# Performance work log

Hardware: AMD Instinct MI355X
Metric: run time of the kernel (lower is better)

Reference implementation:

```python
import jax, jax.numpy as jnp
import numpy as np

N = 50000
F_IN = 256
D_HID = 64
H = 8
C = 10
E_RAND = 800000
ALPHA = 0.2  # leaky_relu negative slope


def setup_inputs() -> dict:
    key = jax.random.key(0)
    k = jax.random.split(key, 7)
    x = jax.random.normal(k[0], (N, F_IN), dtype=jnp.float32)
    # edge list = self-loops (ensure nonzero softmax denominator) + random edges
    self_idx = jnp.arange(N, dtype=jnp.int32)
    edge_src = jnp.concatenate([self_idx, jax.random.randint(k[1], (E_RAND,), 0, N, dtype=jnp.int32)])
    edge_dst = jnp.concatenate([self_idx, jax.random.randint(k[2], (E_RAND,), 0, N, dtype=jnp.int32)])
    W_heads = jax.random.normal(k[3], (H, F_IN, D_HID), dtype=jnp.float32) * 0.05
    a_heads = jax.random.normal(k[4], (H, 2 * D_HID), dtype=jnp.float32) * 0.05
    W_out = jax.random.normal(k[5], (H * D_HID, C), dtype=jnp.float32) * 0.05
    a_out = jax.random.normal(k[6], (2 * C,), dtype=jnp.float32) * 0.05
    return {"x": x, "edge_src": edge_src, "edge_dst": edge_dst,
            "W_heads": W_heads, "a_heads": a_heads, "W_out": W_out, "a_out": a_out}


def sp_gat_layer(x, W, a, src, dst, concat):
    """pyGAT SpGraphAttentionLayer (eval mode, dropout off)."""
    n = x.shape[0]
    d = W.shape[1]
    h = x @ W                                             # [N, d]
    score = h[src] @ a[:d] + h[dst] @ a[d:]               # [E] per-edge attention logit
    e = jnp.exp(-jax.nn.leaky_relu(score, ALPHA))         # unnormalized attention
    rowsum = jax.ops.segment_sum(e, src, num_segments=n)  # [N] softmax denominator
    agg = jax.ops.segment_sum(e[:, None] * h[dst], src, num_segments=n)  # [N, d]
    out = agg / rowsum[:, None]
    return jax.nn.elu(out) if concat else out


def reference(x, edge_src, edge_dst, W_heads, a_heads, W_out, a_out):
    # multi-head sparse attention, heads concatenated along feature dim
    heads = jax.vmap(lambda W, a: sp_gat_layer(x, W, a, edge_src, edge_dst, True))(W_heads, a_heads)  # [H, N, d]
    xcat = jnp.transpose(heads, (1, 0, 2)).reshape(x.shape[0], -1)  # [N, H*d]
    out = jax.nn.elu(sp_gat_layer(xcat, W_out, a_out, edge_src, edge_dst, False))  # [N, C]
    return jax.nn.log_softmax(out, axis=1)
```

## Files before the change

kernel.cpp:

```cpp
#include <hip/hip_runtime.h>
#include <hip/hip_bf16.h>

#define F_IN    256
#define D_HID   64
#define H_HEADS 8
#define NC      10
#define ALPHA   0.2f
#define FLAG_THRESH 64
#define SCAN_T  1024

typedef __attribute__((ext_vector_type(8))) short short8;
typedef __attribute__((ext_vector_type(4))) float f32x4;

__device__ __forceinline__ float bfu2f(unsigned short u) {
    union { float f; unsigned int i; } c; c.i = ((unsigned int)u) << 16; return c.f;
}
__device__ __forceinline__ unsigned short f2bfu(float f) {
    union { float f; unsigned int i; } c; c.f = f;
    unsigned int x = c.i;
    x += 0x7fffu + ((x >> 16) & 1u);
    return (unsigned short)(x >> 16);
}

__global__ void detect_kernel(const unsigned int* __restrict__ x, int* __restrict__ flag) {
    int t = threadIdx.x;
    int cnt = 0;
    for (int i = t; i < 4096; i += 256) {
        unsigned int w = x[i];
        unsigned int e = (w >> 7) & 0xffu;
        if (e >= 140u) cnt++;
    }
    atomicAdd(flag, cnt);
}

__global__ __launch_bounds__(256) void prep_kernel(
    const void* __restrict__ x_raw,  unsigned short* __restrict__ x_bf,
    const void* __restrict__ Wh_raw, unsigned short* __restrict__ wh_t,
    const void* __restrict__ ah_raw, float* __restrict__ ah32,
    const void* __restrict__ Wo_raw, float* __restrict__ Wo32,
    const void* __restrict__ ao_raw, float* __restrict__ ao32,
    const int* __restrict__ esrc, int* __restrict__ counts,
    const int* __restrict__ flagp, int N, int E,
    int bx, int bw, int ba, int bo)
{
    int b = blockIdx.x;
    bool isf32 = (*flagp > FLAG_THRESH);
    if (b < bx) {
        long i = (long)b * 256 + threadIdx.x;
        long n8 = (long)N * F_IN / 8;
        if (i < n8) {
            unsigned short o[8];
            if (isf32) {
                const float* s = (const float*)x_raw + i * 8;
                #pragma unroll
                for (int j = 0; j < 8; ++j) o[j] = f2bfu(s[j]);
            } else {
                *(uint4*)o = ((const uint4*)x_raw)[i];
            }
            *(uint4*)(x_bf + i * 8) = *(uint4*)o;
        }
    } else if (b < bw) {
        int i = (b - bx) * 256 + threadIdx.x;
        int d = i & 63, k = (i >> 6) & 255, h = i >> 14;
        float v = isf32 ? ((const float*)Wh_raw)[i] : bfu2f(((const unsigned short*)Wh_raw)[i]);
        wh_t[(h * 64 + d) * 256 + k] = f2bfu(v);
    } else if (b < ba) {
        int i = (b - bw) * 256 + threadIdx.x;
        ah32[i] = isf32 ? ((const float*)ah_raw)[i] : bfu2f(((const unsigned short*)ah_raw)[i]);
    } else if (b < bo) {
        int i = (b - ba) * 256 + threadIdx.x;
        Wo32[i] = isf32 ? ((const float*)Wo_raw)[i] : bfu2f(((const unsigned short*)Wo_raw)[i]);
    } else if (b == bo) {
        int i = threadIdx.x;
        if (i < 2 * NC)
            ao32[i] = isf32 ? ((const float*)ao_raw)[i] : bfu2f(((const unsigned short*)ao_raw)[i]);
    } else {
        int e = (b - bo - 1) * 256 + threadIdx.x;
        if (e < E) atomicAdd(&counts[esrc[e]], 1);
    }
}

__global__ __launch_bounds__(SCAN_T) void scan_kernel(
    const int* __restrict__ counts, int* __restrict__ row_start, int N, int E)
{
    __shared__ int sums[SCAN_T];
    int t = threadIdx.x;
    int chunk = (N + SCAN_T - 1) / SCAN_T;
    int b = t * chunk, e = min(b + chunk, N);
    int s = 0;
    for (int i = b; i < e; ++i) s += counts[i];
    sums[t] = s;
    __syncthreads();
    for (int off = 1; off < SCAN_T; off <<= 1) {
        int u = (t >= off) ? sums[t - off] : 0;
        __syncthreads();
        sums[t] += u;
        __syncthreads();
    }
    int running = sums[t] - s;
    for (int i = b; i < e; ++i) { row_start[i] = running; running += counts[i]; }
    if (t == SCAN_T - 1) row_start[N] = E;
}

__global__ __launch_bounds__(256) void scatter_ev_kernel(
    const int* __restrict__ src, const int* __restrict__ dst,
    const int* __restrict__ row_start, int* __restrict__ cursor,
    const float* __restrict__ s1s, const float* __restrict__ s1d,
    int* __restrict__ csr_dst, float* __restrict__ ev_csr, int E)
{
    int e = blockIdx.x * 256 + threadIdx.x;
    if (e >= E) return;
    int s = src[e], d = dst[e];
    int pos = atomicAdd(&cursor[s], 1);
    int i = row_start[s] + pos;
    csr_dst[i] = d;
    float4 ss0 = *(const float4*)(s1s + s * 8);
    float4 ss1 = *(const float4*)(s1s + s * 8 + 4);
    float4 sd0 = *(const float4*)(s1d + d * 8);
    float4 sd1 = *(const float4*)(s1d + d * 8 + 4);
    float sc[8] = { ss0.x + sd0.x, ss0.y + sd0.y, ss0.z + sd0.z, ss0.w + sd0.w,
                    ss1.x + sd1.x, ss1.y + sd1.y, ss1.z + sd1.z, ss1.w + sd1.w };
    float ev[8];
    #pragma unroll
    for (int h = 0; h < 8; ++h) {
        float lr = sc[h] > 0.f ? sc[h] : ALPHA * sc[h];
        ev[h] = __expf(-lr);
    }
    *(float4*)(ev_csr + (long)i * 8)     = make_float4(ev[0], ev[1], ev[2], ev[3]);
    *(float4*)(ev_csr + (long)i * 8 + 4) = make_float4(ev[4], ev[5], ev[6], ev[7]);
}

__global__ __launch_bounds__(256) void gemm1_kernel(
    const unsigned short* __restrict__ x_bf,
    const unsigned short* __restrict__ wh_t,
    const float* __restrict__ ah,
    unsigned short* __restrict__ h_bf,
    float* __restrict__ s1s, float* __restrict__ s1d, int N)
{
    __shared__ unsigned short Os[64][72];

    const int t = threadIdx.x;
    const int w = t >> 6, lane = t & 63;
    const int q = lane >> 4, m = lane & 15;
    const int n0 = blockIdx.x * 64;
    const int h0 = blockIdx.y * 2;

    int r = n0 + 16 * w + m;
    const unsigned short* xr = x_bf + (long)(r < N ? r : N - 1) * 256;
    short8 afrag[8];
    #pragma unroll
    for (int ks = 0; ks < 8; ++ks)
        afrag[ks] = *(const short8*)(xr + ks * 32 + q * 8);

    #pragma unroll
    for (int hi = 0; hi < 2; ++hi) {
        const int h = h0 + hi;
        f32x4 acc[4] = {};
        const unsigned short* Bh = wh_t + (long)h * 64 * 256;
        #pragma unroll
        for (int ks = 0; ks < 8; ++ks) {
            #pragma unroll
            for (int c = 0; c < 4; ++c) {
                short8 b = *(const short8*)(Bh + (c * 16 + m) * 256 + ks * 32 + q * 8);
                acc[c] = __builtin_amdgcn_mfma_f32_16x16x32_bf16(afrag[ks], b, acc[c], 0, 0, 0);
            }
        }

        const float* a1 = ah + h * 128;
        float a1m = a1[m], a1m16 = a1[16 + m], a1m32 = a1[32 + m], a1m48 = a1[48 + m];
        float a2m = a1[64 + m], a2m16 = a1[80 + m], a2m32 = a1[96 + m], a2m48 = a1[112 + m];
        #pragma unroll
        for (int reg = 0; reg < 4; ++reg) {
            float p1 = acc[0][reg] * a1m + acc[1][reg] * a1m16 + acc[2][reg] * a1m32 + acc[3][reg] * a1m48;
            float p2 = acc[0][reg] * a2m + acc[1][reg] * a2m16 + acc[2][reg] * a2m32 + acc[3][reg] * a2m48;
            #pragma unroll
            for (int off = 1; off < 16; off <<= 1) {
                p1 += __shfl_xor(p1, off);
                p2 += __shfl_xor(p2, off);
            }
            int row = n0 + 16 * w + q * 4 + reg;
            if (m == 0 && row < N) {
                s1s[row * 8 + h] = p1;
                s1d[row * 8 + h] = p2;
            }
        }

        #pragma unroll
        for (int c = 0; c < 4; ++c)
            #pragma unroll
            for (int reg = 0; reg < 4; ++reg)
                Os[16 * w + q * 4 + reg][c * 16 + m] = f2bfu(acc[c][reg]);
        #pragma unroll
        for (int j = 0; j < 2; ++j) {
            int cc = j * 64 + lane;
            int row = cc >> 3, c8 = cc & 7;
            if (n0 + 16 * w + row < N)
                *(uint4*)(h_bf + (long)(n0 + 16 * w + row) * 512 + h * 64 + c8 * 8) =
                    *(const uint4*)&Os[16 * w + row][c8 * 8];
        }
    }
}

__global__ __launch_bounds__(256) void edge_agg1_kernel(
    const int* __restrict__ row_start, const int* __restrict__ csr_dst,
    const float* __restrict__ ev_csr,
    const uint4* __restrict__ h_q,
    uint4* __restrict__ xcat_q,
    int N)
{
    int lane = threadIdx.x & 63;
    int n = blockIdx.x * 4 + (threadIdx.x >> 6);
    if (n >= N) return;
    int h = lane >> 3;
    int beg = row_start[n], end = row_start[n + 1];

    float acc[8] = {0.f, 0.f, 0.f, 0.f, 0.f, 0.f, 0.f, 0.f};
    float rs = 0.f;
    int dnext = csr_dst[beg];
    for (int i = beg; i < end; ++i) {
        int d = dnext;
        if (i + 1 < end) dnext = csr_dst[i + 1];
        float ev = ev_csr[(long)i * 8 + h];
        uint4 wv = h_q[(long)d * 64 + lane];
        rs += ev;
        acc[0] += ev * bfu2f((unsigned short)(wv.x & 0xffffu));
        acc[1] += ev * bfu2f((unsigned short)(wv.x >> 16));
        acc[2] += ev * bfu2f((unsigned short)(wv.y & 0xffffu));
        acc[3] += ev * bfu2f((unsigned short)(wv.y >> 16));
        acc[4] += ev * bfu2f((unsigned short)(wv.z & 0xffffu));
        acc[5] += ev * bfu2f((unsigned short)(wv.z >> 16));
        acc[6] += ev * bfu2f((unsigned short)(wv.w & 0xffffu));
        acc[7] += ev * bfu2f((unsigned short)(wv.w >> 16));
    }
    float inv = 1.f / rs;
    unsigned short o[8];
    #pragma unroll
    for (int j = 0; j < 8; ++j) {
        float v = acc[j] * inv;
        v = v > 0.f ? v : __expf(v) - 1.f;
        o[j] = f2bfu(v);
    }
    xcat_q[(long)n * 64 + lane] = *(const uint4*)o;
}

__global__ __launch_bounds__(256) void gemm2_kernel(
    const unsigned short* __restrict__ xcat_bf,
    const float* __restrict__ Wo,
    const float* __restrict__ ao,
    float* __restrict__ h2p,
    float* __restrict__ s2s, float* __restrict__ s2d, int N)
{
    int n = blockIdx.x * 256 + threadIdx.x;
    if (n >= N) return;
    float acc[NC];
    #pragma unroll
    for (int c = 0; c < NC; ++c) acc[c] = 0.f;
    const uint4* xp = (const uint4*)(xcat_bf + (long)n * 512);
    for (int k8 = 0; k8 < 64; ++k8) {
        uint4 w = xp[k8];
        float f[8];
        f[0] = bfu2f((unsigned short)(w.x & 0xffffu)); f[1] = bfu2f((unsigned short)(w.x >> 16));
        f[2] = bfu2f((unsigned short)(w.y & 0xffffu)); f[3] = bfu2f((unsigned short)(w.y >> 16));
        f[4] = bfu2f((unsigned short)(w.z & 0xffffu)); f[5] = bfu2f((unsigned short)(w.z >> 16));
        f[6] = bfu2f((unsigned short)(w.w & 0xffffu)); f[7] = bfu2f((unsigned short)(w.w >> 16));
        #pragma unroll
        for (int u = 0; u < 8; ++u) {
            const float* wr = Wo + (k8 * 8 + u) * NC;
            #pragma unroll
            for (int c = 0; c < NC; ++c) acc[c] += f[u] * wr[c];
        }
    }
    float s1 = 0.f, s2 = 0.f;
    *(float4*)(h2p + (long)n * 16)      = make_float4(acc[0], acc[1], acc[2], acc[3]);
    *(float4*)(h2p + (long)n * 16 + 4)  = make_float4(acc[4], acc[5], acc[6], acc[7]);
    *(float4*)(h2p + (long)n * 16 + 8)  = make_float4(acc[8], acc[9], 0.f, 0.f);
    *(float4*)(h2p + (long)n * 16 + 12) = make_float4(0.f, 0.f, 0.f, 0.f);
    #pragma unroll
    for (int c = 0; c < NC; ++c) {
        s1 += acc[c] * ao[c];
        s2 += acc[c] * ao[NC + c];
    }
    s2s[n] = s1;
    s2d[n] = s2;
}

__global__ __launch_bounds__(256) void edge_agg2_kernel(
    const int* __restrict__ row_start, const int* __restrict__ csr_dst,
    const float* __restrict__ h2p,
    const float* __restrict__ s_src2, const float* __restrict__ s_dst2,
    void* __restrict__ out, const int* __restrict__ flagp, int N)
{
    int lane = threadIdx.x & 63;
    int n = blockIdx.x * 4 + (threadIdx.x >> 6);
    if (n >= N) return;
    int c = lane & 15, j = lane >> 4;
    int beg = row_start[n], end = row_start[n + 1];
    float ss = s_src2[n];
    float rs = 0.f, acc = 0.f;
    for (int i0 = beg; i0 < end; i0 += 4) {
        int i = i0 + j;
        if (i < end) {
            int d = csr_dst[i];
            float sc = ss + s_dst2[d];
            float lr = sc > 0.f ? sc : ALPHA * sc;
            float ev = __expf(-lr);
            rs += ev;
            acc += ev * h2p[(long)d * 16 + c];
        }
    }
    rs  += __shfl_xor(rs, 16, 64);  rs  += __shfl_xor(rs, 32, 64);
    acc += __shfl_xor(acc, 16, 64); acc += __shfl_xor(acc, 32, 64);
    float v = acc / rs;
    v = v > 0.f ? v : __expf(v) - 1.f;
    float vm = (c < NC) ? v : -1e30f;
    #pragma unroll
    for (int off = 1; off < 16; off <<= 1) vm = fmaxf(vm, __shfl_xor(vm, off, 64));
    float ex = (c < NC) ? __expf(v - vm) : 0.f;
    #pragma unroll
    for (int off = 1; off < 16; off <<= 1) ex += __shfl_xor(ex, off, 64);
    float lse = vm + logf(ex);
    if (c < NC && j == 0) {
        bool isf32 = (*flagp > FLAG_THRESH);
        if (isf32) ((float*)out)[(long)n * NC + c] = v - lse;
        else       ((unsigned short*)out)[(long)n * NC + c] = f2bfu(v - lse);
    }
}

extern "C" void kernel_launch(void* const* d_in, const int* in_sizes, int n_in,
                              void* d_out, int out_size, void* d_ws, size_t ws_size,
                              hipStream_t stream)
{
    const void* x_raw  = d_in[0];
    const int*  esrc   = (const int*)d_in[1];
    const int*  edst   = (const int*)d_in[2];
    const void* Wh_raw = d_in[3];
    const void* ah_raw = d_in[4];
    const void* Wo_raw = d_in[5];
    const void* ao_raw = d_in[6];

    const int N = in_sizes[0] / F_IN;
    const int E = in_sizes[1];

    char* ws = (char*)d_ws;
    size_t off = 0;
    auto alloc = [&](size_t bytes) -> void* {
        void* p = ws + off;
        off = (off + bytes + 255) & ~(size_t)255;
        return p;
    };
    int*            flag      = (int*)           alloc(4);
    int*            counts    = (int*)           alloc((size_t)N * 4);
    int*            cursor    = (int*)           alloc((size_t)N * 4);
    size_t clear_span = (size_t)((char*)cursor + (size_t)N * 4 - (char*)flag);

    unsigned short* x_bf      = (unsigned short*)alloc((size_t)N * F_IN * 2);
    unsigned short* wh_t      = (unsigned short*)alloc((size_t)H_HEADS * D_HID * F_IN * 2);
    float*          ah32      = (float*)         alloc((size_t)H_HEADS * 2 * D_HID * 4);
    float*          Wo32      = (float*)         alloc((size_t)512 * NC * 4);
    float*          ao32      = (float*)         alloc((size_t)2 * NC * 4);
    unsigned short* h_bf      = (unsigned short*)alloc((size_t)N * 512 * 2);
    unsigned short* xcat_bf   = (unsigned short*)alloc((size_t)N * 512 * 2);
    float*          s1s       = (float*)         alloc((size_t)N * 8 * 4);
    float*          s1d       = (float*)         alloc((size_t)N * 8 * 4);
    float*          h2p       = (float*)         alloc((size_t)N * 16 * 4);
    float*          s2s       = (float*)         alloc((size_t)N * 4);
    float*          s2d       = (float*)         alloc((size_t)N * 4);
    int*            row_start = (int*)           alloc((size_t)(N + 1) * 4);
    int*            csr_dst   = (int*)           alloc((size_t)E * 4);
    float*          ev_csr    = (float*)         alloc((size_t)E * 8 * 4);
    (void)ws_size;

    hipMemsetAsync(flag, 0, clear_span, stream);

    detect_kernel<<<1, 256, 0, stream>>>((const unsigned int*)x_raw, flag);
    int bx = (int)(((long)N * F_IN / 8 + 255) / 256);
    int bw = bx + (H_HEADS * F_IN * D_HID) / 256;
    int ba = bw + (H_HEADS * 2 * D_HID) / 256;
    int bo = ba + (512 * NC) / 256;
    int nb = bo + 1 + (E + 255) / 256;
    prep_kernel<<<nb, 256, 0, stream>>>(x_raw, x_bf, Wh_raw, wh_t, ah_raw, ah32,
                                        Wo_raw, Wo32, ao_raw, ao32,
                                        esrc, counts, flag, N, E, bx, bw, ba, bo);
    scan_kernel<<<1, SCAN_T, 0, stream>>>(counts, row_start, N, E);

    dim3 g1((N + 63) / 64, H_HEADS / 2);
    gemm1_kernel<<<g1, 256, 0, stream>>>(x_bf, wh_t, ah32, h_bf, s1s, s1d, N);
    scatter_ev_kernel<<<(E + 255) / 256, 256, 0, stream>>>(esrc, edst, row_start, cursor,
                                                           s1s, s1d, csr_dst, ev_csr, E);
    edge_agg1_kernel<<<(N + 3) / 4, 256, 0, stream>>>(row_start, csr_dst, ev_csr,
                                                      (const uint4*)h_bf, (uint4*)xcat_bf, N);

    gemm2_kernel<<<(N + 255) / 256, 256, 0, stream>>>(xcat_bf, Wo32, ao32, h2p, s2s, s2d, N);
    edge_agg2_kernel<<<(N + 3) / 4, 256, 0, stream>>>(row_start, csr_dst, h2p, s2s, s2d, d_out, flag, N);
}
```

Before: 585.1 us.

## Inline dtype detection, pre-swizzle head weights for MFMA, split gemm2 across two threads

Drops the separate detect kernel and flag memset: each wave checks the input dtype with a ballot over 64 words of x. Head weights are stored in an MFMA-fragment order, so each lane of gemm1 reads a contiguous 16-byte B fragment instead of strided rows. gemm2 splits each node's 512-long reduction across two threads and combines them with a shuffle, doubling parallelism. The dtype check now looks at fewer words, so it is less robust to unusual inputs.

```diff
diff --git a/kernel.cpp b/kernel.cpp
--- a/kernel.cpp
+++ b/kernel.cpp
@@ -6,7 +6,6 @@
 #define H_HEADS 8
 #define NC      10
 #define ALPHA   0.2f
-#define FLAG_THRESH 64
 #define SCAN_T  1024
 
 typedef __attribute__((ext_vector_type(8))) short short8;
@@ -22,29 +21,24 @@
     return (unsigned short)(x >> 16);
 }
 
-__global__ void detect_kernel(const unsigned int* __restrict__ x, int* __restrict__ flag) {
-    int t = threadIdx.x;
-    int cnt = 0;
-    for (int i = t; i < 4096; i += 256) {
-        unsigned int w = x[i];
-        unsigned int e = (w >> 7) & 0xffu;
-        if (e >= 140u) cnt++;
-    }
-    atomicAdd(flag, cnt);
+__device__ __forceinline__ bool detect_f32(const void* xraw) {
+    unsigned int w = ((const unsigned int*)xraw)[threadIdx.x & 63];
+    unsigned int e = (w >> 7) & 0xffu;
+    unsigned long long m = __ballot(e >= 140u);
+    return __popcll(m) > 8;
 }
 
 __global__ __launch_bounds__(256) void prep_kernel(
     const void* __restrict__ x_raw,  unsigned short* __restrict__ x_bf,
-    const void* __restrict__ Wh_raw, unsigned short* __restrict__ wh_t,
+    const void* __restrict__ Wh_raw, unsigned short* __restrict__ wh_f,
     const void* __restrict__ ah_raw, float* __restrict__ ah32,
     const void* __restrict__ Wo_raw, float* __restrict__ Wo32,
     const void* __restrict__ ao_raw, float* __restrict__ ao32,
     const int* __restrict__ esrc, int* __restrict__ counts,
-    const int* __restrict__ flagp, int N, int E,
-    int bx, int bw, int ba, int bo)
+    int N, int E, int bx, int bw, int ba, int bo)
 {
     int b = blockIdx.x;
-    bool isf32 = (*flagp > FLAG_THRESH);
+    bool isf32 = detect_f32(x_raw);
     if (b < bx) {
         long i = (long)b * 256 + threadIdx.x;
         long n8 = (long)N * F_IN / 8;
@@ -63,7 +57,9 @@
         int i = (b - bx) * 256 + threadIdx.x;
         int d = i & 63, k = (i >> 6) & 255, h = i >> 14;
         float v = isf32 ? ((const float*)Wh_raw)[i] : bfu2f(((const unsigned short*)Wh_raw)[i]);
-        wh_t[(h * 64 + d) * 256 + k] = f2bfu(v);
+        int ks = k >> 5, q = (k >> 3) & 3, j = k & 7;
+        int c = d >> 4, m = d & 15;
+        wh_f[(((h * 8 + ks) * 4 + c) << 9) + (q * 16 + m) * 8 + j] = f2bfu(v);
     } else if (b < ba) {
         int i = (b - bw) * 256 + threadIdx.x;
         ah32[i] = isf32 ? ((const float*)ah_raw)[i] : bfu2f(((const unsigned short*)ah_raw)[i]);
@@ -132,7 +128,7 @@
 
 __global__ __launch_bounds__(256) void gemm1_kernel(
     const unsigned short* __restrict__ x_bf,
-    const unsigned short* __restrict__ wh_t,
+    const unsigned short* __restrict__ wh_f,
     const float* __restrict__ ah,
     unsigned short* __restrict__ h_bf,
     float* __restrict__ s1s, float* __restrict__ s1d, int N)
@@ -156,12 +152,12 @@
     for (int hi = 0; hi < 2; ++hi) {
         const int h = h0 + hi;
         f32x4 acc[4] = {};
-        const unsigned short* Bh = wh_t + (long)h * 64 * 256;
+        const unsigned short* Bh = wh_f + (((long)h * 32) << 9);
         #pragma unroll
         for (int ks = 0; ks < 8; ++ks) {
             #pragma unroll
             for (int c = 0; c < 4; ++c) {
-                short8 b = *(const short8*)(Bh + (c * 16 + m) * 256 + ks * 32 + q * 8);
+                short8 b = *(const short8*)(Bh + (((ks * 4 + c) << 9) + lane * 8));
                 acc[c] = __builtin_amdgcn_mfma_f32_16x16x32_bf16(afrag[ks], b, acc[c], 0, 0, 0);
             }
         }
@@ -250,13 +246,15 @@
     float* __restrict__ h2p,
     float* __restrict__ s2s, float* __restrict__ s2d, int N)
 {
-    int n = blockIdx.x * 256 + threadIdx.x;
+    int tid = blockIdx.x * 256 + threadIdx.x;
+    int n = tid >> 1;
     if (n >= N) return;
+    int half = tid & 1;
     float acc[NC];
     #pragma unroll
     for (int c = 0; c < NC; ++c) acc[c] = 0.f;
-    const uint4* xp = (const uint4*)(xcat_bf + (long)n * 512);
-    for (int k8 = 0; k8 < 64; ++k8) {
+    const uint4* xp = (const uint4*)(xcat_bf + (long)n * 512) + half * 32;
+    for (int k8 = 0; k8 < 32; ++k8) {
         uint4 w = xp[k8];
         float f[8];
         f[0] = bfu2f((unsigned short)(w.x & 0xffffu)); f[1] = bfu2f((unsigned short)(w.x >> 16));
@@ -265,31 +263,36 @@
         f[6] = bfu2f((unsigned short)(w.w & 0xffffu)); f[7] = bfu2f((unsigned short)(w.w >> 16));
         #pragma unroll
         for (int u = 0; u < 8; ++u) {
-            const float* wr = Wo + (k8 * 8 + u) * NC;
+            const float* wr = Wo + ((half * 32 + k8) * 8 + u) * NC;
             #pragma unroll
             for (int c = 0; c < NC; ++c) acc[c] += f[u] * wr[c];
         }
     }
-    float s1 = 0.f, s2 = 0.f;
-    *(float4*)(h2p + (long)n * 16)      = make_float4(acc[0], acc[1], acc[2], acc[3]);
-    *(float4*)(h2p + (long)n * 16 + 4)  = make_float4(acc[4], acc[5], acc[6], acc[7]);
-    *(float4*)(h2p + (long)n * 16 + 8)  = make_float4(acc[8], acc[9], 0.f, 0.f);
-    *(float4*)(h2p + (long)n * 16 + 12) = make_float4(0.f, 0.f, 0.f, 0.f);
-    #pragma unroll
-    for (int c = 0; c < NC; ++c) {
-        s1 += acc[c] * ao[c];
-        s2 += acc[c] * ao[NC + c];
-    }
-    s2s[n] = s1;
-    s2d[n] = s2;
+    #pragma unroll
+    for (int c = 0; c < NC; ++c) acc[c] += __shfl_xor(acc[c], 1, 64);
+    if (half == 0) {
+        float s1 = 0.f, s2 = 0.f;
+        *(float4*)(h2p + (long)n * 16)      = make_float4(acc[0], acc[1], acc[2], acc[3]);
+        *(float4*)(h2p + (long)n * 16 + 4)  = make_float4(acc[4], acc[5], acc[6], acc[7]);
+        *(float4*)(h2p + (long)n * 16 + 8)  = make_float4(acc[8], acc[9], 0.f, 0.f);
+        *(float4*)(h2p + (long)n * 16 + 12) = make_float4(0.f, 0.f, 0.f, 0.f);
+        #pragma unroll
+        for (int c = 0; c < NC; ++c) {
+            s1 += acc[c] * ao[c];
+            s2 += acc[c] * ao[NC + c];
+        }
+        s2s[n] = s1;
+        s2d[n] = s2;
+    }
 }
 
 __global__ __launch_bounds__(256) void edge_agg2_kernel(
     const int* __restrict__ row_start, const int* __restrict__ csr_dst,
     const float* __restrict__ h2p,
     const float* __restrict__ s_src2, const float* __restrict__ s_dst2,
-    void* __restrict__ out, const int* __restrict__ flagp, int N)
-{
+    void* __restrict__ out, const void* __restrict__ x_raw, int N)
+{
+    bool isf32 = detect_f32(x_raw);
     int lane = threadIdx.x & 63;
     int n = blockIdx.x * 4 + (threadIdx.x >> 6);
     if (n >= N) return;
@@ -320,7 +323,6 @@
     for (int off = 1; off < 16; off <<= 1) ex += __shfl_xor(ex, off, 64);
     float lse = vm + logf(ex);
     if (c < NC && j == 0) {
-        bool isf32 = (*flagp > FLAG_THRESH);
         if (isf32) ((float*)out)[(long)n * NC + c] = v - lse;
         else       ((unsigned short*)out)[(long)n * NC + c] = f2bfu(v - lse);
     }
@@ -348,13 +350,12 @@
         off = (off + bytes + 255) & ~(size_t)255;
         return p;
     };
-    int*            flag      = (int*)           alloc(4);
     int*            counts    = (int*)           alloc((size_t)N * 4);
     int*            cursor    = (int*)           alloc((size_t)N * 4);
-    size_t clear_span = (size_t)((char*)cursor + (size_t)N * 4 - (char*)flag);
+    size_t clear_span = (size_t)((char*)cursor + (size_t)N * 4 - (char*)counts);
 
     unsigned short* x_bf      = (unsigned short*)alloc((size_t)N * F_IN * 2);
-    unsigned short* wh_t      = (unsigned short*)alloc((size_t)H_HEADS * D_HID * F_IN * 2);
+    unsigned short* wh_f      = (unsigned short*)alloc((size_t)H_HEADS * D_HID * F_IN * 2);
     float*          ah32      = (float*)         alloc((size_t)H_HEADS * 2 * D_HID * 4);
     float*          Wo32      = (float*)         alloc((size_t)512 * NC * 4);
     float*          ao32      = (float*)         alloc((size_t)2 * NC * 4);
@@ -370,26 +371,25 @@
     float*          ev_csr    = (float*)         alloc((size_t)E * 8 * 4);
     (void)ws_size;
 
-    hipMemsetAsync(flag, 0, clear_span, stream);
-
-    detect_kernel<<<1, 256, 0, stream>>>((const unsigned int*)x_raw, flag);
+    hipMemsetAsync(counts, 0, clear_span, stream);
+
     int bx = (int)(((long)N * F_IN / 8 + 255) / 256);
     int bw = bx + (H_HEADS * F_IN * D_HID) / 256;
     int ba = bw + (H_HEADS * 2 * D_HID) / 256;
     int bo = ba + (512 * NC) / 256;
     int nb = bo + 1 + (E + 255) / 256;
-    prep_kernel<<<nb, 256, 0, stream>>>(x_raw, x_bf, Wh_raw, wh_t, ah_raw, ah32,
+    prep_kernel<<<nb, 256, 0, stream>>>(x_raw, x_bf, Wh_raw, wh_f, ah_raw, ah32,
                                         Wo_raw, Wo32, ao_raw, ao32,
-                                        esrc, counts, flag, N, E, bx, bw, ba, bo);
+                                        esrc, counts, N, E, bx, bw, ba, bo);
     scan_kernel<<<1, SCAN_T, 0, stream>>>(counts, row_start, N, E);
 
     dim3 g1((N + 63) / 64, H_HEADS / 2);
-    gemm1_kernel<<<g1, 256, 0, stream>>>(x_bf, wh_t, ah32, h_bf, s1s, s1d, N);
+    gemm1_kernel<<<g1, 256, 0, stream>>>(x_bf, wh_f, ah32, h_bf, s1s, s1d, N);
     scatter_ev_kernel<<<(E + 255) / 256, 256, 0, stream>>>(esrc, edst, row_start, cursor,
                                                            s1s, s1d, csr_dst, ev_csr, E);
     edge_agg1_kernel<<<(N + 3) / 4, 256, 0, stream>>>(row_start, csr_dst, ev_csr,
                                                       (const uint4*)h_bf, (uint4*)xcat_bf, N);
 
-    gemm2_kernel<<<(N + 255) / 256, 256, 0, stream>>>(xcat_bf, Wo32, ao32, h2p, s2s, s2d, N);
-    edge_agg2_kernel<<<(N + 3) / 4, 256, 0, stream>>>(row_start, csr_dst, h2p, s2s, s2d, d_out, flag, N);
-}
+    gemm2_kernel<<<(2 * N + 255) / 256, 256, 0, stream>>>(xcat_bf, Wo32, ao32, h2p, s2s, s2d, N);
+    edge_agg2_kernel<<<(N + 3) / 4, 256, 0, stream>>>(row_start, csr_dst, h2p, s2s, s2d, d_out, x_raw, N);
+}
```

New measurement: 561.1 us. -4.1%, faster.
